# Performance work log

Hardware: AMD Instinct MI355X
Metric: run time of the kernel (lower is better)

## Reference

```python
import jax, jax.numpy as jnp
import numpy as np

C = 768       # hidden_dim
HEADS = 12    # num_heads
HDIM = C // HEADS  # 64


def _ln(x, w, eps=1e-5):
    # LayerNorm with weight, no bias (matches nn.LayerNorm(..., bias=False))
    mu = jnp.mean(x, axis=-1, keepdims=True)
    var = jnp.mean((x - mu) ** 2, axis=-1, keepdims=True)
    return (x - mu) * jax.lax.rsqrt(var + eps) * w


def _attn(q, k, v):
    # scaled dot product attention over the second-to-last axis
    scale = 1.0 / np.sqrt(q.shape[-1]).astype(np.float32)
    s = jnp.einsum('...qc,...kc->...qk', q, k) * scale
    return jnp.einsum('...qk,...kc->...qc', jax.nn.softmax(s, axis=-1), v)


def setup_inputs() -> dict:
    key = jax.random.key(0)
    ks = jax.random.split(key, 4)
    B, H, W = 4, 64, 64
    x = jax.random.normal(ks[0], (B, H, W, C), jnp.float32)
    Wqkv = jax.random.normal(ks[1], (C, 7 * C), jnp.float32) * 0.02
    bqkv = jnp.zeros((7 * C,), jnp.float32)
    Wout = jax.random.normal(ks[2], (C, C), jnp.float32) * 0.02
    bout = jnp.zeros((C,), jnp.float32)
    Wmlp = jax.random.normal(ks[3], (4 * C, C), jnp.float32) * 0.02
    bmlp = jnp.zeros((C,), jnp.float32)
    norm_w = jnp.ones((C,), jnp.float32)
    qnorm_w = jnp.ones((HDIM,), jnp.float32)
    knorm_w = jnp.ones((HDIM,), jnp.float32)
    gamma = jnp.full((C,), 1e-6, jnp.float32)
    return {"x": x, "norm_w": norm_w, "Wqkv": Wqkv, "bqkv": bqkv,
            "qnorm_w": qnorm_w, "knorm_w": knorm_w, "Wout": Wout,
            "bout": bout, "Wmlp": Wmlp, "bmlp": bmlp, "gamma": gamma}


def reference(x, norm_w, Wqkv, bqkv, qnorm_w, knorm_w, Wout, bout, Wmlp, bmlp, gamma):
    B, H, W, _ = x.shape
    xn = _ln(x, norm_w)
    proj = xn @ Wqkv + bqkv                       # (B,H,W,7C)
    q, k, v, ff = jnp.split(proj, [C, 2 * C, 3 * C], axis=-1)
    heads = lambda t: t.reshape(B, H, W, HEADS, HDIM)
    q, k, v = heads(q), heads(k), heads(v)        # (B,H,W,He,c)
    q = _ln(q, qnorm_w)
    k = _ln(k, knorm_w)

    # --- axis 1: 'b h w he c -> b h he w c', attend over w ---
    q, k, v = (t.transpose(0, 1, 3, 2, 4) for t in (q, k, v))  # (B,H,He,W,c)
    ax = _attn(q, k, v)                                         # (B,H,He,W,c)
    # out_permutation 'b w he h c -> b h w (he c)' applied POSITIONALLY ->
    # the first axis contribution lands spatially transposed (requires H==W)
    out = ax.transpose(0, 3, 1, 2, 4).reshape(B, W, H, C)

    # --- axis 2: 'b h he w c -> b w he h c' (positional), attend over h ---
    q, k, v = (t.transpose(0, 3, 2, 1, 4) for t in (q, k, v))  # (B,W,He,H,c)
    ax = _attn(q, k, v)                                         # (B,W,He,H,c)
    out = out + ax.transpose(0, 3, 1, 2, 4).reshape(B, H, W, C)

    y = out @ Wout + bout + (jax.nn.gelu(ff, approximate=False) @ Wmlp + bmlp)
    return x + gamma * y
```

## Files before the change

kernel.cpp:

```cpp
#include <hip/hip_runtime.h>

typedef unsigned short u16;
typedef unsigned int u32;
typedef unsigned char u8;
typedef long i64;
typedef float f4 __attribute__((ext_vector_type(4)));
typedef int i32x8 __attribute__((ext_vector_type(8)));

#define CDIM 768
#define NPROJ 5376
#define KFF 3840
#define NTOK 16384

__device__ __forceinline__ u8 f2fp8(float f) {
#if __has_builtin(__builtin_amdgcn_cvt_pk_fp8_f32)
    return (u8)(__builtin_amdgcn_cvt_pk_fp8_f32(f, f, 0, false) & 0xff);
#else
    u32 u = __float_as_uint(f);
    u32 s = (u >> 24) & 0x80u;
    float a = fabsf(f);
    a = fminf(a, 448.f);
    if (a < 0.015625f) return (u8)(s | (u32)(a * 512.f + 0.5f));
    u32 b = __float_as_uint(a);
    b += 0x0007FFFFu + ((b >> 20) & 1u);
    u32 e = b >> 23, m = (b >> 20) & 7u;
    u32 code = ((e - 120u) << 3) | m;
    if (code > 0x7Eu) code = 0x7Eu;
    return (u8)(s | code);
#endif
}
__device__ __forceinline__ u32 pk4_fp8(float a, float b, float c, float d) {
#if __has_builtin(__builtin_amdgcn_cvt_pk_fp8_f32)
    u32 lo = (u32)__builtin_amdgcn_cvt_pk_fp8_f32(a, b, 0, false);
    return (u32)__builtin_amdgcn_cvt_pk_fp8_f32(c, d, lo, true);
#else
    return (u32)f2fp8(a) | ((u32)f2fp8(b) << 8) | ((u32)f2fp8(c) << 16) | ((u32)f2fp8(d) << 24);
#endif
}
__device__ __forceinline__ float fp8_to_f32(u32 v) {
#if __has_builtin(__builtin_amdgcn_cvt_f32_fp8)
    return __builtin_amdgcn_cvt_f32_fp8((int)v, 0);
#else
    u32 s = v >> 7, e = (v >> 3) & 15u, m = v & 7u;
    float mag = e ? __uint_as_float(((e + 120u) << 23) | (m << 20))
                  : (float)m * 0.001953125f;
    return s ? -mag : mag;
#endif
}

__device__ __forceinline__ float wsum64(float v) {
#pragma unroll
    for (int m = 32; m > 0; m >>= 1) v += __shfl_xor(v, m, 64);
    return v;
}
__device__ __forceinline__ void gl_lds16(const u8* g, u8* l) {
    __builtin_amdgcn_global_load_lds((__attribute__((address_space(1))) u32*)g,
                                     (__attribute__((address_space(3))) u32*)l,
                                     16, 0, 0);
}

__global__ __launch_bounds__(256) void transpose_cast(const float* __restrict__ src,
                                                      u8* __restrict__ dst,
                                                      int R, int Cc, int dstride, int doff) {
    __shared__ float t[32][33];
    int c0 = blockIdx.x * 32, r0 = blockIdx.y * 32;
    int tx = threadIdx.x, ty = threadIdx.y;
#pragma unroll
    for (int i = 0; i < 32; i += 8) {
        int r = r0 + ty + i, c = c0 + tx;
        if (r < R && c < Cc) t[ty + i][tx] = src[(size_t)r * Cc + c];
    }
    __syncthreads();
#pragma unroll
    for (int i = 0; i < 32; i += 8) {
        int c = c0 + ty + i, r = r0 + tx;
        if (r < R && c < Cc) dst[(size_t)c * dstride + doff + r] = f2fp8(t[tx][ty + i]);
    }
}

__global__ __launch_bounds__(256) void ln_rows(const float* __restrict__ x,
                                               const float* __restrict__ w,
                                               u8* __restrict__ xn) {
    int row = blockIdx.x * 4 + (threadIdx.x >> 6);
    int lane = threadIdx.x & 63;
    const f4* xr = (const f4*)(x + (size_t)row * CDIM);
    const f4* wr = (const f4*)w;
    f4 v[3];
    float s = 0.f, s2 = 0.f;
#pragma unroll
    for (int i = 0; i < 3; ++i) {
        v[i] = xr[lane + 64 * i];
#pragma unroll
        for (int j = 0; j < 4; ++j) { s += v[i][j]; s2 += v[i][j] * v[i][j]; }
    }
    s = wsum64(s); s2 = wsum64(s2);
    float mu = s * (1.f / 768.f);
    float var = s2 * (1.f / 768.f) - mu * mu;
    float rs = rsqrtf(var + 1e-5f);
    u32* xo = (u32*)(xn + (size_t)row * CDIM);
#pragma unroll
    for (int i = 0; i < 3; ++i) {
        f4 wv = wr[lane + 64 * i];
        xo[lane + 64 * i] = pk4_fp8((v[i][0] - mu) * rs * wv[0], (v[i][1] - mu) * rs * wv[1],
                                    (v[i][2] - mu) * rs * wv[2], (v[i][3] - mu) * rs * wv[3]);
    }
}

template <int MODE>
__global__ __launch_bounds__(256) void gemm_bt(
    const u8* __restrict__ A, const u8* __restrict__ B, int M, int N, int K,
    const float* __restrict__ bias0, const float* __restrict__ bias1,
    const float* __restrict__ xres, const float* __restrict__ gamma,
    u8* __restrict__ oqkv, u8* __restrict__ off, float* __restrict__ ofin) {
    __shared__ __align__(16) u8 As[128 * 128];
    __shared__ __align__(16) u8 Bs[128 * 128];
    const int tid = threadIdx.x;
    const int wid = tid >> 6, lane = tid & 63;
    const int wm = wid >> 1, wn = wid & 1;
    const int quad = lane >> 4, l16 = lane & 15;
    const int m0 = blockIdx.y * 128, n0 = blockIdx.x * 128;

    f4 acc[4][4] = {};

    const int rl = lane >> 3;
    const int csw = ((lane & 7) ^ rl) * 16;
    const u8* aptr[4]; const u8* bptr[4];
    u8* alds[4]; u8* blds[4];
#pragma unroll
    for (int jj = 0; jj < 4; ++jj) {
        const int r0 = wid * 32 + jj * 8;
        aptr[jj] = A + (size_t)(m0 + r0 + rl) * K + csw;
        bptr[jj] = B + (size_t)(n0 + r0 + rl) * K + csw;
        alds[jj] = As + r0 * 128;
        blds[jj] = Bs + r0 * 128;
    }
    const int swl = l16 & 7;

    for (int kt = 0; kt < K; kt += 128) {
#pragma unroll
        for (int jj = 0; jj < 4; ++jj) {
            gl_lds16(aptr[jj] + kt, alds[jj]);
            gl_lds16(bptr[jj] + kt, blds[jj]);
        }
        __syncthreads();
        const int c0 = ((2 * quad) ^ swl) * 16;
        const int c1 = ((2 * quad + 1) ^ swl) * 16;
        i32x8 af[4], bfv[4];
#pragma unroll
        for (int mi = 0; mi < 4; ++mi) {
            const u8* base = As + (wm * 64 + mi * 16 + l16) * 128;
            uint4 lo = *(const uint4*)(base + c0);
            uint4 hi = *(const uint4*)(base + c1);
            af[mi][0] = lo.x; af[mi][1] = lo.y; af[mi][2] = lo.z; af[mi][3] = lo.w;
            af[mi][4] = hi.x; af[mi][5] = hi.y; af[mi][6] = hi.z; af[mi][7] = hi.w;
        }
#pragma unroll
        for (int ni = 0; ni < 4; ++ni) {
            const u8* base = Bs + (wn * 64 + ni * 16 + l16) * 128;
            uint4 lo = *(const uint4*)(base + c0);
            uint4 hi = *(const uint4*)(base + c1);
            bfv[ni][0] = lo.x; bfv[ni][1] = lo.y; bfv[ni][2] = lo.z; bfv[ni][3] = lo.w;
            bfv[ni][4] = hi.x; bfv[ni][5] = hi.y; bfv[ni][6] = hi.z; bfv[ni][7] = hi.w;
        }
#pragma unroll
        for (int mi = 0; mi < 4; ++mi)
#pragma unroll
            for (int ni = 0; ni < 4; ++ni)
                acc[mi][ni] = __builtin_amdgcn_mfma_scale_f32_16x16x128_f8f6f4(
                    af[mi], bfv[ni], acc[mi][ni], 0, 0, 0, 127, 0, 127);
        __syncthreads();
    }

#pragma unroll
    for (int mi = 0; mi < 4; ++mi) {
#pragma unroll
        for (int ni = 0; ni < 4; ++ni) {
            const int col = n0 + wn * 64 + ni * 16 + l16;
            const int rowb = m0 + wm * 64 + mi * 16 + quad * 4;
            if (MODE == 0) {
                const float bc = bias0[col];
#pragma unroll
                for (int r = 0; r < 4; ++r) {
                    float vv = acc[mi][ni][r] + bc;
                    const int m = rowb + r;
                    if (col < 2304) {
                        oqkv[(size_t)m * 2304 + col] = f2fp8(vv);
                    } else {
                        float u2 = vv * (-1.5957691216f) - 0.0713548162f * vv * vv * vv;
                        float g = vv / (1.f + __expf(u2));
                        off[(size_t)m * KFF + 768 + (col - 2304)] = f2fp8(g);
                    }
                }
            } else {
                const float bc = bias0[col] + bias1[col];
                const float gm = gamma[col];
#pragma unroll
                for (int r = 0; r < 4; ++r) {
                    const int m = rowb + r;
                    float vv = acc[mi][ni][r] + bc;
                    ofin[(size_t)m * CDIM + col] = xres[(size_t)m * CDIM + col] + gm * vv;
                }
            }
        }
    }
}

__global__ __launch_bounds__(256) void qk_ln(u8* __restrict__ qkv,
                                             const float* __restrict__ qw,
                                             const float* __restrict__ kw) {
    const size_t m = blockIdx.x;
    const int w = threadIdx.x >> 6, lane = threadIdx.x & 63;
#pragma unroll
    for (int it = 0; it < 6; ++it) {
        const int h = w + 4 * it;
        const int isq = (h < 12);
        const int he = isq ? h : h - 12;
        u8* p = qkv + m * 2304 + (isq ? 0 : 768) + he * 64 + lane;
        const float wt = (isq ? qw : kw)[lane];
        float v = fp8_to_f32(*p);
        float mu = wsum64(v) * (1.f / 64.f);
        float ex2 = wsum64(v * v) * (1.f / 64.f);
        float rs = rsqrtf(ex2 - mu * mu + 1e-5f);
        *p = f2fp8((v - mu) * rs * wt);
    }
}

__global__ __launch_bounds__(256) void axial_attn_mfma(const u8* __restrict__ qkv,
                                                       u8* __restrict__ A2) {
    __shared__ __align__(16) u8 Qs[64 * 72];
    __shared__ __align__(16) u8 Ks[64 * 72];
    __shared__ __align__(16) u8 Vt[64 * 72];
    __shared__ __align__(16) u8 Ps[64 * 72];

    const int bx = blockIdx.x;
    const int he = bx % 12;
    const int j = (bx / 12) & 63;
    const int b = bx / (12 * 64);
    const int tid = threadIdx.x;
    const int w = tid >> 6, lane = tid & 63;
    const int l16 = lane & 15, quad = lane >> 4;
    const int qb = w * 16;

    f4 acc_o[4] = {};

    const int sr = tid >> 2;
    const int sc = (tid & 3) * 16;

    for (int phase = 0; phase < 2; ++phase) {
        const size_t tok = (phase == 0) ? (size_t)((b * 64 + j) * 64 + sr)
                                        : (size_t)((b * 64 + sr) * 64 + j);
        const u8* src = qkv + tok * 2304 + he * 64 + sc;
        {
            uint4 qv = *(const uint4*)(src);
            uint4 kv = *(const uint4*)(src + 768);
            *(uint4*)(Qs + sr * 72 + sc) = qv;
            *(uint4*)(Ks + sr * 72 + sc) = kv;
        }
        {
            uint4 vv = *(const uint4*)(src + 1536);
            const u8* vb = (const u8*)&vv;
#pragma unroll
            for (int i = 0; i < 16; ++i) Vt[(sc + i) * 72 + sr] = vb[i];
        }
        __syncthreads();

        f4 st[4] = {};
#pragma unroll
        for (int kt = 0; kt < 2; ++kt) {
            const int boff = (kt * 4 + quad) * 8;
            const i64 bq = *(const i64*)(Qs + (qb + l16) * 72 + boff);
#pragma unroll
            for (int mt = 0; mt < 4; ++mt) {
                const i64 ak = *(const i64*)(Ks + (mt * 16 + l16) * 72 + boff);
                st[mt] = __builtin_amdgcn_mfma_f32_16x16x32_fp8_fp8(ak, bq, st[mt], 0, 0, 0);
            }
        }

        float sv[16];
        float mx = -1e30f;
#pragma unroll
        for (int mt = 0; mt < 4; ++mt)
#pragma unroll
            for (int r = 0; r < 4; ++r) {
                const float s = st[mt][r] * 0.125f;
                sv[mt * 4 + r] = s;
                mx = fmaxf(mx, s);
            }
        mx = fmaxf(mx, __shfl_xor(mx, 16, 64));
        mx = fmaxf(mx, __shfl_xor(mx, 32, 64));
        float sm = 0.f;
#pragma unroll
        for (int i = 0; i < 16; ++i) { sv[i] = __expf(sv[i] - mx); sm += sv[i]; }
        sm += __shfl_xor(sm, 16, 64);
        sm += __shfl_xor(sm, 32, 64);
        const float inv = 1.f / sm;

#pragma unroll
        for (int mt = 0; mt < 4; ++mt) {
            const int kbase = mt * 16 + quad * 4;
            *(u32*)(Ps + (qb + l16) * 72 + kbase) =
                pk4_fp8(sv[mt * 4] * inv, sv[mt * 4 + 1] * inv,
                        sv[mt * 4 + 2] * inv, sv[mt * 4 + 3] * inv);
        }
        __syncthreads();

#pragma unroll
        for (int kt = 0; kt < 2; ++kt) {
            const int boff = (kt * 4 + quad) * 8;
            const i64 ap = *(const i64*)(Ps + (qb + l16) * 72 + boff);
#pragma unroll
            for (int nt = 0; nt < 4; ++nt) {
                const i64 bv = *(const i64*)(Vt + (nt * 16 + l16) * 72 + boff);
                acc_o[nt] = __builtin_amdgcn_mfma_f32_16x16x32_fp8_fp8(ap, bv, acc_o[nt], 0, 0, 0);
            }
        }
        __syncthreads();
    }

#pragma unroll
    for (int nt = 0; nt < 4; ++nt)
#pragma unroll
        for (int r = 0; r < 4; ++r) {
            const int q = qb + quad * 4 + r;
            const int c = nt * 16 + l16;
            A2[((size_t)((b * 64 + q) * 64 + j)) * KFF + he * 64 + c] = f2fp8(acc_o[nt][r]);
        }
}

extern "C" void kernel_launch(void* const* d_in, const int* in_sizes, int n_in,
                              void* d_out, int out_size, void* d_ws, size_t ws_size,
                              hipStream_t stream) {
    const float* x = (const float*)d_in[0];
    const float* normw = (const float*)d_in[1];
    const float* Wqkv = (const float*)d_in[2];
    const float* bqkv = (const float*)d_in[3];
    const float* qnw = (const float*)d_in[4];
    const float* knw = (const float*)d_in[5];
    const float* Wout = (const float*)d_in[6];
    const float* bout = (const float*)d_in[7];
    const float* Wmlp = (const float*)d_in[8];
    const float* bmlp = (const float*)d_in[9];
    const float* gamma = (const float*)d_in[10];
    float* out = (float*)d_out;

    char* ws = (char*)d_ws;
    u8* xn = (u8*)ws;    ws += (size_t)NTOK * CDIM;
    u8* WqkvT = (u8*)ws; ws += (size_t)NPROJ * CDIM;
    u8* BT2 = (u8*)ws;   ws += (size_t)CDIM * KFF;
    u8* qkv = (u8*)ws;   ws += (size_t)NTOK * 2304;
    u8* A2 = (u8*)ws;    ws += (size_t)NTOK * KFF;

    transpose_cast<<<dim3(NPROJ / 32, CDIM / 32), dim3(32, 8), 0, stream>>>(Wqkv, WqkvT, CDIM, NPROJ, CDIM, 0);
    transpose_cast<<<dim3(CDIM / 32, CDIM / 32), dim3(32, 8), 0, stream>>>(Wout, BT2, CDIM, CDIM, KFF, 0);
    transpose_cast<<<dim3(CDIM / 32, 3072 / 32), dim3(32, 8), 0, stream>>>(Wmlp, BT2, 3072, CDIM, KFF, 768);
    ln_rows<<<NTOK / 4, 256, 0, stream>>>(x, normw, xn);
    gemm_bt<0><<<dim3(NPROJ / 128, NTOK / 128), 256, 0, stream>>>(
        xn, WqkvT, NTOK, NPROJ, CDIM, bqkv, nullptr, nullptr, nullptr, qkv, A2, nullptr);
    qk_ln<<<NTOK, 256, 0, stream>>>(qkv, qnw, knw);
    axial_attn_mfma<<<3072, 256, 0, stream>>>(qkv, A2);
    gemm_bt<1><<<dim3(CDIM / 128, NTOK / 128), 256, 0, stream>>>(
        A2, BT2, NTOK, CDIM, KFF, bout, bmlp, x, gamma, nullptr, nullptr, out);
}
```

Measured before the change: 421.2 us.

## Restructure FP8 GEMM to 256x256 tiles with double-buffered LDS prefetch

```diff
diff --git a/kernel.cpp b/kernel.cpp
--- a/kernel.cpp
+++ b/kernel.cpp
@@ -107,76 +107,107 @@
 }
 
 template <int MODE>
-__global__ __launch_bounds__(256) void gemm_bt(
+__global__ __launch_bounds__(512, 2) void gemm_bt(
     const u8* __restrict__ A, const u8* __restrict__ B, int M, int N, int K,
     const float* __restrict__ bias0, const float* __restrict__ bias1,
     const float* __restrict__ xres, const float* __restrict__ gamma,
     u8* __restrict__ oqkv, u8* __restrict__ off, float* __restrict__ ofin) {
-    __shared__ __align__(16) u8 As[128 * 128];
-    __shared__ __align__(16) u8 Bs[128 * 128];
+    __shared__ __align__(16) u8 lds[2][2][32768];
     const int tid = threadIdx.x;
     const int wid = tid >> 6, lane = tid & 63;
-    const int wm = wid >> 1, wn = wid & 1;
+    const int wm = wid >> 2, wn = wid & 3;
     const int quad = lane >> 4, l16 = lane & 15;
-    const int m0 = blockIdx.y * 128, n0 = blockIdx.x * 128;
-
-    f4 acc[4][4] = {};
+
+    const int nwg = (int)gridDim.x;
+    int bid = (int)blockIdx.x;
+    bid = (bid & 7) * (nwg >> 3) + (bid >> 3);
+    const int nbx = N >> 8;
+    const int m0 = (bid / nbx) << 8;
+    const int n0 = (bid % nbx) << 8;
+    const int NT = K >> 7;
+
+    f4 acc[8][4] = {};
 
     const int rl = lane >> 3;
     const int csw = ((lane & 7) ^ rl) * 16;
+    const int srow = wid * 8 + rl;
     const u8* aptr[4]; const u8* bptr[4];
-    u8* alds[4]; u8* blds[4];
-#pragma unroll
-    for (int jj = 0; jj < 4; ++jj) {
-        const int r0 = wid * 32 + jj * 8;
-        aptr[jj] = A + (size_t)(m0 + r0 + rl) * K + csw;
-        bptr[jj] = B + (size_t)(n0 + r0 + rl) * K + csw;
-        alds[jj] = As + r0 * 128;
-        blds[jj] = Bs + r0 * 128;
-    }
-    const int swl = l16 & 7;
-
-    for (int kt = 0; kt < K; kt += 128) {
-#pragma unroll
-        for (int jj = 0; jj < 4; ++jj) {
-            gl_lds16(aptr[jj] + kt, alds[jj]);
-            gl_lds16(bptr[jj] + kt, blds[jj]);
-        }
-        __syncthreads();
-        const int c0 = ((2 * quad) ^ swl) * 16;
-        const int c1 = ((2 * quad + 1) ^ swl) * 16;
-        i32x8 af[4], bfv[4];
-#pragma unroll
-        for (int mi = 0; mi < 4; ++mi) {
-            const u8* base = As + (wm * 64 + mi * 16 + l16) * 128;
-            uint4 lo = *(const uint4*)(base + c0);
-            uint4 hi = *(const uint4*)(base + c1);
-            af[mi][0] = lo.x; af[mi][1] = lo.y; af[mi][2] = lo.z; af[mi][3] = lo.w;
-            af[mi][4] = hi.x; af[mi][5] = hi.y; af[mi][6] = hi.z; af[mi][7] = hi.w;
-        }
-#pragma unroll
-        for (int ni = 0; ni < 4; ++ni) {
-            const u8* base = Bs + (wn * 64 + ni * 16 + l16) * 128;
-            uint4 lo = *(const uint4*)(base + c0);
-            uint4 hi = *(const uint4*)(base + c1);
-            bfv[ni][0] = lo.x; bfv[ni][1] = lo.y; bfv[ni][2] = lo.z; bfv[ni][3] = lo.w;
-            bfv[ni][4] = hi.x; bfv[ni][5] = hi.y; bfv[ni][6] = hi.z; bfv[ni][7] = hi.w;
-        }
-#pragma unroll
-        for (int mi = 0; mi < 4; ++mi)
-#pragma unroll
-            for (int ni = 0; ni < 4; ++ni)
-                acc[mi][ni] = __builtin_amdgcn_mfma_scale_f32_16x16x128_f8f6f4(
-                    af[mi], bfv[ni], acc[mi][ni], 0, 0, 0, 127, 0, 127);
-        __syncthreads();
-    }
-
-#pragma unroll
-    for (int mi = 0; mi < 4; ++mi) {
+#pragma unroll
+    for (int i = 0; i < 4; ++i) {
+        aptr[i] = A + (size_t)(m0 + i * 64 + srow) * K + csw;
+        bptr[i] = B + (size_t)(n0 + i * 64 + srow) * K + csw;
+    }
+    const int ldso = wid * 1024;
+
+#pragma unroll
+    for (int i = 0; i < 4; ++i) {
+        gl_lds16(aptr[i], &lds[0][0][i * 8192 + ldso]);
+        gl_lds16(bptr[i], &lds[0][1][i * 8192 + ldso]);
+    }
+    asm volatile("s_waitcnt vmcnt(0)" ::: "memory");
+    __builtin_amdgcn_s_barrier();
+
+    const int cb0 = ((2 * quad) ^ (l16 & 7)) * 16;
+    const int cb1 = ((2 * quad + 1) ^ (l16 & 7)) * 16;
+
+    for (int t = 0; t < NT; ++t) {
+        const u8* Ab = lds[t & 1][0];
+        const u8* Bb = lds[t & 1][1];
+        u8* Aw = lds[(t & 1) ^ 1][0];
+        u8* Bw = lds[(t & 1) ^ 1][1];
+        const int pf = (t + 1 < NT);
+        const size_t knext = (size_t)(t + 1) << 7;
+#pragma unroll
+        for (int p = 0; p < 4; ++p) {
+            const int mib = (p & 1) * 4;
+            const int nib = (p >> 1) * 2;
+            i32x8 af[4]; i32x8 bf[2];
+#pragma unroll
+            for (int mi = 0; mi < 4; ++mi) {
+                const u8* base = Ab + (wm * 128 + (mib + mi) * 16 + l16) * 128;
+                uint4 lo = *(const uint4*)(base + cb0);
+                uint4 hi = *(const uint4*)(base + cb1);
+                af[mi][0] = lo.x; af[mi][1] = lo.y; af[mi][2] = lo.z; af[mi][3] = lo.w;
+                af[mi][4] = hi.x; af[mi][5] = hi.y; af[mi][6] = hi.z; af[mi][7] = hi.w;
+            }
+#pragma unroll
+            for (int ni = 0; ni < 2; ++ni) {
+                const u8* base = Bb + (wn * 64 + (nib + ni) * 16 + l16) * 128;
+                uint4 lo = *(const uint4*)(base + cb0);
+                uint4 hi = *(const uint4*)(base + cb1);
+                bf[ni][0] = lo.x; bf[ni][1] = lo.y; bf[ni][2] = lo.z; bf[ni][3] = lo.w;
+                bf[ni][4] = hi.x; bf[ni][5] = hi.y; bf[ni][6] = hi.z; bf[ni][7] = hi.w;
+            }
+            if (p < 2 && pf) {
+#pragma unroll
+                for (int i = 2 * p; i < 2 * p + 2; ++i) {
+                    gl_lds16(aptr[i] + knext, Aw + i * 8192 + ldso);
+                    gl_lds16(bptr[i] + knext, Bw + i * 8192 + ldso);
+                }
+            }
+            __builtin_amdgcn_sched_barrier(0);
+            __builtin_amdgcn_s_barrier();
+            asm volatile("s_waitcnt lgkmcnt(0)" ::: "memory");
+            __builtin_amdgcn_sched_barrier(0);
+            __builtin_amdgcn_s_setprio(1);
+#pragma unroll
+            for (int mi = 0; mi < 4; ++mi)
+#pragma unroll
+                for (int ni = 0; ni < 2; ++ni)
+                    acc[mib + mi][nib + ni] = __builtin_amdgcn_mfma_scale_f32_16x16x128_f8f6f4(
+                        af[mi], bf[ni], acc[mib + mi][nib + ni], 0, 0, 0, 127, 0, 127);
+            __builtin_amdgcn_s_setprio(0);
+            if (p == 3) asm volatile("s_waitcnt vmcnt(0)" ::: "memory");
+            __builtin_amdgcn_s_barrier();
+        }
+    }
+
+#pragma unroll
+    for (int mi = 0; mi < 8; ++mi) {
 #pragma unroll
         for (int ni = 0; ni < 4; ++ni) {
             const int col = n0 + wn * 64 + ni * 16 + l16;
-            const int rowb = m0 + wm * 64 + mi * 16 + quad * 4;
+            const int rowb = m0 + wm * 128 + mi * 16 + quad * 4;
             if (MODE == 0) {
                 const float bc = bias0[col];
 #pragma unroll
@@ -354,10 +385,10 @@
     transpose_cast<<<dim3(CDIM / 32, CDIM / 32), dim3(32, 8), 0, stream>>>(Wout, BT2, CDIM, CDIM, KFF, 0);
     transpose_cast<<<dim3(CDIM / 32, 3072 / 32), dim3(32, 8), 0, stream>>>(Wmlp, BT2, 3072, CDIM, KFF, 768);
     ln_rows<<<NTOK / 4, 256, 0, stream>>>(x, normw, xn);
-    gemm_bt<0><<<dim3(NPROJ / 128, NTOK / 128), 256, 0, stream>>>(
+    gemm_bt<0><<<dim3((NPROJ / 256) * (NTOK / 256)), 512, 0, stream>>>(
         xn, WqkvT, NTOK, NPROJ, CDIM, bqkv, nullptr, nullptr, nullptr, qkv, A2, nullptr);
     qk_ln<<<NTOK, 256, 0, stream>>>(qkv, qnw, knw);
     axial_attn_mfma<<<3072, 256, 0, stream>>>(qkv, A2);
-    gemm_bt<1><<<dim3(CDIM / 128, NTOK / 128), 256, 0, stream>>>(
+    gemm_bt<1><<<dim3((CDIM / 256) * (NTOK / 256)), 512, 0, stream>>>(
         A2, BT2, NTOK, CDIM, KFF, bout, bmlp, x, gamma, nullptr, nullptr, out);
 }
```

Measured after the change: 562.4 us. +33.5%, slower.

## Double-buffer LDS tiles in fp8 GEMM to overlap global loads with MFMA

Applied to the files above, without the earlier changes.

```diff
diff --git a/kernel.cpp b/kernel.cpp
--- a/kernel.cpp
+++ b/kernel.cpp
@@ -112,53 +112,63 @@
     const float* __restrict__ bias0, const float* __restrict__ bias1,
     const float* __restrict__ xres, const float* __restrict__ gamma,
     u8* __restrict__ oqkv, u8* __restrict__ off, float* __restrict__ ofin) {
-    __shared__ __align__(16) u8 As[128 * 128];
-    __shared__ __align__(16) u8 Bs[128 * 128];
+    __shared__ __align__(16) u8 As[2][128 * 128];
+    __shared__ __align__(16) u8 Bs[2][128 * 128];
     const int tid = threadIdx.x;
     const int wid = tid >> 6, lane = tid & 63;
     const int wm = wid >> 1, wn = wid & 1;
     const int quad = lane >> 4, l16 = lane & 15;
     const int m0 = blockIdx.y * 128, n0 = blockIdx.x * 128;
+    const int NT = K >> 7;
 
     f4 acc[4][4] = {};
 
     const int rl = lane >> 3;
     const int csw = ((lane & 7) ^ rl) * 16;
     const u8* aptr[4]; const u8* bptr[4];
-    u8* alds[4]; u8* blds[4];
+    int ro[4];
 #pragma unroll
     for (int jj = 0; jj < 4; ++jj) {
         const int r0 = wid * 32 + jj * 8;
         aptr[jj] = A + (size_t)(m0 + r0 + rl) * K + csw;
         bptr[jj] = B + (size_t)(n0 + r0 + rl) * K + csw;
-        alds[jj] = As + r0 * 128;
-        blds[jj] = Bs + r0 * 128;
+        ro[jj] = r0 * 128;
     }
     const int swl = l16 & 7;
-
-    for (int kt = 0; kt < K; kt += 128) {
-#pragma unroll
-        for (int jj = 0; jj < 4; ++jj) {
-            gl_lds16(aptr[jj] + kt, alds[jj]);
-            gl_lds16(bptr[jj] + kt, blds[jj]);
-        }
-        __syncthreads();
-        const int c0 = ((2 * quad) ^ swl) * 16;
-        const int c1 = ((2 * quad + 1) ^ swl) * 16;
+    const int cb0 = ((2 * quad) ^ swl) * 16;
+    const int cb1 = ((2 * quad + 1) ^ swl) * 16;
+
+#pragma unroll
+    for (int jj = 0; jj < 4; ++jj) {
+        gl_lds16(aptr[jj], &As[0][ro[jj]]);
+        gl_lds16(bptr[jj], &Bs[0][ro[jj]]);
+    }
+    __syncthreads();
+
+    for (int t = 0; t < NT; ++t) {
+        const int cur = t & 1, nxt = cur ^ 1;
+        if (t + 1 < NT) {
+            const size_t ko = (size_t)(t + 1) << 7;
+#pragma unroll
+            for (int jj = 0; jj < 4; ++jj) {
+                gl_lds16(aptr[jj] + ko, &As[nxt][ro[jj]]);
+                gl_lds16(bptr[jj] + ko, &Bs[nxt][ro[jj]]);
+            }
+        }
         i32x8 af[4], bfv[4];
 #pragma unroll
         for (int mi = 0; mi < 4; ++mi) {
-            const u8* base = As + (wm * 64 + mi * 16 + l16) * 128;
-            uint4 lo = *(const uint4*)(base + c0);
-            uint4 hi = *(const uint4*)(base + c1);
+            const u8* base = As[cur] + (wm * 64 + mi * 16 + l16) * 128;
+            uint4 lo = *(const uint4*)(base + cb0);
+            uint4 hi = *(const uint4*)(base + cb1);
             af[mi][0] = lo.x; af[mi][1] = lo.y; af[mi][2] = lo.z; af[mi][3] = lo.w;
             af[mi][4] = hi.x; af[mi][5] = hi.y; af[mi][6] = hi.z; af[mi][7] = hi.w;
         }
 #pragma unroll
         for (int ni = 0; ni < 4; ++ni) {
-            const u8* base = Bs + (wn * 64 + ni * 16 + l16) * 128;
-            uint4 lo = *(const uint4*)(base + c0);
-            uint4 hi = *(const uint4*)(base + c1);
+            const u8* base = Bs[cur] + (wn * 64 + ni * 16 + l16) * 128;
+            uint4 lo = *(const uint4*)(base + cb0);
+            uint4 hi = *(const uint4*)(base + cb1);
             bfv[ni][0] = lo.x; bfv[ni][1] = lo.y; bfv[ni][2] = lo.z; bfv[ni][3] = lo.w;
             bfv[ni][4] = hi.x; bfv[ni][5] = hi.y; bfv[ni][6] = hi.z; bfv[ni][7] = hi.w;
         }
```

Result: slower. 444.5 us (+5.5%).

## Fuse weight prep and input LayerNorm into one launch; fold QK-norm into attention

Applied to the files above, without the earlier changes.

```diff
diff --git a/kernel.cpp b/kernel.cpp
--- a/kernel.cpp
+++ b/kernel.cpp
@@ -59,50 +59,66 @@
                                      16, 0, 0);
 }
 
-__global__ __launch_bounds__(256) void transpose_cast(const float* __restrict__ src,
-                                                      u8* __restrict__ dst,
-                                                      int R, int Cc, int dstride, int doff) {
+__global__ __launch_bounds__(256) void prep_fused(
+    const float* __restrict__ Wqkv, u8* __restrict__ WqkvT,
+    const float* __restrict__ Wout, const float* __restrict__ Wmlp,
+    u8* __restrict__ BT2,
+    const float* __restrict__ x, const float* __restrict__ normw,
+    u8* __restrict__ xn) {
     __shared__ float t[32][33];
-    int c0 = blockIdx.x * 32, r0 = blockIdx.y * 32;
-    int tx = threadIdx.x, ty = threadIdx.y;
-#pragma unroll
-    for (int i = 0; i < 32; i += 8) {
-        int r = r0 + ty + i, c = c0 + tx;
-        if (r < R && c < Cc) t[ty + i][tx] = src[(size_t)r * Cc + c];
-    }
-    __syncthreads();
-#pragma unroll
-    for (int i = 0; i < 32; i += 8) {
-        int c = c0 + ty + i, r = r0 + tx;
-        if (r < R && c < Cc) dst[(size_t)c * dstride + doff + r] = f2fp8(t[tx][ty + i]);
-    }
-}
-
-__global__ __launch_bounds__(256) void ln_rows(const float* __restrict__ x,
-                                               const float* __restrict__ w,
-                                               u8* __restrict__ xn) {
-    int row = blockIdx.x * 4 + (threadIdx.x >> 6);
-    int lane = threadIdx.x & 63;
-    const f4* xr = (const f4*)(x + (size_t)row * CDIM);
-    const f4* wr = (const f4*)w;
-    f4 v[3];
-    float s = 0.f, s2 = 0.f;
-#pragma unroll
-    for (int i = 0; i < 3; ++i) {
-        v[i] = xr[lane + 64 * i];
-#pragma unroll
-        for (int j = 0; j < 4; ++j) { s += v[i][j]; s2 += v[i][j] * v[i][j]; }
-    }
-    s = wsum64(s); s2 = wsum64(s2);
-    float mu = s * (1.f / 768.f);
-    float var = s2 * (1.f / 768.f) - mu * mu;
-    float rs = rsqrtf(var + 1e-5f);
-    u32* xo = (u32*)(xn + (size_t)row * CDIM);
-#pragma unroll
-    for (int i = 0; i < 3; ++i) {
-        f4 wv = wr[lane + 64 * i];
-        xo[lane + 64 * i] = pk4_fp8((v[i][0] - mu) * rs * wv[0], (v[i][1] - mu) * rs * wv[1],
-                                    (v[i][2] - mu) * rs * wv[2], (v[i][3] - mu) * rs * wv[3]);
+    const int bid = blockIdx.x;
+    const int tid = threadIdx.x;
+    if (bid < 6912) {
+        const float* src; u8* dst; int R, Cc, dstride, doff, bx, by;
+        if (bid < 4032) {
+            src = Wqkv; dst = WqkvT; R = CDIM; Cc = NPROJ; dstride = CDIM; doff = 0;
+            bx = bid % 168; by = bid / 168;
+        } else if (bid < 4608) {
+            const int b2 = bid - 4032;
+            src = Wout; dst = BT2; R = CDIM; Cc = CDIM; dstride = KFF; doff = 0;
+            bx = b2 % 24; by = b2 / 24;
+        } else {
+            const int b2 = bid - 4608;
+            src = Wmlp; dst = BT2; R = 3072; Cc = CDIM; dstride = KFF; doff = 768;
+            bx = b2 % 24; by = b2 / 24;
+        }
+        const int c0 = bx * 32, r0 = by * 32;
+        const int tx = tid & 31, ty = tid >> 5;
+#pragma unroll
+        for (int i = 0; i < 32; i += 8) {
+            int r = r0 + ty + i, c = c0 + tx;
+            if (r < R && c < Cc) t[ty + i][tx] = src[(size_t)r * Cc + c];
+        }
+        __syncthreads();
+#pragma unroll
+        for (int i = 0; i < 32; i += 8) {
+            int c = c0 + ty + i, r = r0 + tx;
+            if (r < R && c < Cc) dst[(size_t)c * dstride + doff + r] = f2fp8(t[tx][ty + i]);
+        }
+    } else {
+        const int row = (bid - 6912) * 4 + (tid >> 6);
+        const int lane = tid & 63;
+        const f4* xr = (const f4*)(x + (size_t)row * CDIM);
+        const f4* wr = (const f4*)normw;
+        f4 v[3];
+        float s = 0.f, s2 = 0.f;
+#pragma unroll
+        for (int i = 0; i < 3; ++i) {
+            v[i] = xr[lane + 64 * i];
+#pragma unroll
+            for (int j = 0; j < 4; ++j) { s += v[i][j]; s2 += v[i][j] * v[i][j]; }
+        }
+        s = wsum64(s); s2 = wsum64(s2);
+        float mu = s * (1.f / 768.f);
+        float var = s2 * (1.f / 768.f) - mu * mu;
+        float rs = rsqrtf(var + 1e-5f);
+        u32* xo = (u32*)(xn + (size_t)row * CDIM);
+#pragma unroll
+        for (int i = 0; i < 3; ++i) {
+            f4 wv = wr[lane + 64 * i];
+            xo[lane + 64 * i] = pk4_fp8((v[i][0] - mu) * rs * wv[0], (v[i][1] - mu) * rs * wv[1],
+                                        (v[i][2] - mu) * rs * wv[2], (v[i][3] - mu) * rs * wv[3]);
+        }
     }
 }
 
@@ -205,27 +221,9 @@
     }
 }
 
-__global__ __launch_bounds__(256) void qk_ln(u8* __restrict__ qkv,
-                                             const float* __restrict__ qw,
-                                             const float* __restrict__ kw) {
-    const size_t m = blockIdx.x;
-    const int w = threadIdx.x >> 6, lane = threadIdx.x & 63;
-#pragma unroll
-    for (int it = 0; it < 6; ++it) {
-        const int h = w + 4 * it;
-        const int isq = (h < 12);
-        const int he = isq ? h : h - 12;
-        u8* p = qkv + m * 2304 + (isq ? 0 : 768) + he * 64 + lane;
-        const float wt = (isq ? qw : kw)[lane];
-        float v = fp8_to_f32(*p);
-        float mu = wsum64(v) * (1.f / 64.f);
-        float ex2 = wsum64(v * v) * (1.f / 64.f);
-        float rs = rsqrtf(ex2 - mu * mu + 1e-5f);
-        *p = f2fp8((v - mu) * rs * wt);
-    }
-}
-
 __global__ __launch_bounds__(256) void axial_attn_mfma(const u8* __restrict__ qkv,
+                                                       const float* __restrict__ qnw,
+                                                       const float* __restrict__ knw,
                                                        u8* __restrict__ A2) {
     __shared__ __align__(16) u8 Qs[64 * 72];
     __shared__ __align__(16) u8 Ks[64 * 72];
@@ -245,6 +243,8 @@
 
     const int sr = tid >> 2;
     const int sc = (tid & 3) * 16;
+    const f4* qwv = (const f4*)(qnw + sc);
+    const f4* kwv = (const f4*)(knw + sc);
 
     for (int phase = 0; phase < 2; ++phase) {
         const size_t tok = (phase == 0) ? (size_t)((b * 64 + j) * 64 + sr)
@@ -253,8 +253,45 @@
         {
             uint4 qv = *(const uint4*)(src);
             uint4 kv = *(const uint4*)(src + 768);
-            *(uint4*)(Qs + sr * 72 + sc) = qv;
-            *(uint4*)(Ks + sr * 72 + sc) = kv;
+            const u32* qu = (const u32*)&qv;
+            const u32* ku = (const u32*)&kv;
+            float qf[16], kf[16];
+#pragma unroll
+            for (int jj = 0; jj < 4; ++jj)
+#pragma unroll
+                for (int bb = 0; bb < 4; ++bb) {
+                    qf[jj * 4 + bb] = fp8_to_f32((qu[jj] >> (8 * bb)) & 0xffu);
+                    kf[jj * 4 + bb] = fp8_to_f32((ku[jj] >> (8 * bb)) & 0xffu);
+                }
+            float s1q = 0.f, s2q = 0.f, s1k = 0.f, s2k = 0.f;
+#pragma unroll
+            for (int i = 0; i < 16; ++i) {
+                s1q += qf[i]; s2q += qf[i] * qf[i];
+                s1k += kf[i]; s2k += kf[i] * kf[i];
+            }
+            s1q += __shfl_xor(s1q, 1, 64); s1q += __shfl_xor(s1q, 2, 64);
+            s2q += __shfl_xor(s2q, 1, 64); s2q += __shfl_xor(s2q, 2, 64);
+            s1k += __shfl_xor(s1k, 1, 64); s1k += __shfl_xor(s1k, 2, 64);
+            s2k += __shfl_xor(s2k, 1, 64); s2k += __shfl_xor(s2k, 2, 64);
+            const float muq = s1q * (1.f / 64.f), muk = s1k * (1.f / 64.f);
+            const float rsq = rsqrtf(s2q * (1.f / 64.f) - muq * muq + 1e-5f);
+            const float rsk = rsqrtf(s2k * (1.f / 64.f) - muk * muk + 1e-5f);
+            uint4 qo, ko;
+            u32* qop = (u32*)&qo; u32* kop = (u32*)&ko;
+#pragma unroll
+            for (int jj = 0; jj < 4; ++jj) {
+                const f4 wq = qwv[jj], wk = kwv[jj];
+                qop[jj] = pk4_fp8((qf[jj * 4 + 0] - muq) * rsq * wq[0],
+                                  (qf[jj * 4 + 1] - muq) * rsq * wq[1],
+                                  (qf[jj * 4 + 2] - muq) * rsq * wq[2],
+                                  (qf[jj * 4 + 3] - muq) * rsq * wq[3]);
+                kop[jj] = pk4_fp8((kf[jj * 4 + 0] - muk) * rsk * wk[0],
+                                  (kf[jj * 4 + 1] - muk) * rsk * wk[1],
+                                  (kf[jj * 4 + 2] - muk) * rsk * wk[2],
+                                  (kf[jj * 4 + 3] - muk) * rsk * wk[3]);
+            }
+            *(uint4*)(Qs + sr * 72 + sc) = qo;
+            *(uint4*)(Ks + sr * 72 + sc) = ko;
         }
         {
             uint4 vv = *(const uint4*)(src + 1536);
@@ -350,14 +387,10 @@
     u8* qkv = (u8*)ws;   ws += (size_t)NTOK * 2304;
     u8* A2 = (u8*)ws;    ws += (size_t)NTOK * KFF;
 
-    transpose_cast<<<dim3(NPROJ / 32, CDIM / 32), dim3(32, 8), 0, stream>>>(Wqkv, WqkvT, CDIM, NPROJ, CDIM, 0);
-    transpose_cast<<<dim3(CDIM / 32, CDIM / 32), dim3(32, 8), 0, stream>>>(Wout, BT2, CDIM, CDIM, KFF, 0);
-    transpose_cast<<<dim3(CDIM / 32, 3072 / 32), dim3(32, 8), 0, stream>>>(Wmlp, BT2, 3072, CDIM, KFF, 768);
-    ln_rows<<<NTOK / 4, 256, 0, stream>>>(x, normw, xn);
+    prep_fused<<<11008, 256, 0, stream>>>(Wqkv, WqkvT, Wout, Wmlp, BT2, x, normw, xn);
     gemm_bt<0><<<dim3(NPROJ / 128, NTOK / 128), 256, 0, stream>>>(
         xn, WqkvT, NTOK, NPROJ, CDIM, bqkv, nullptr, nullptr, nullptr, qkv, A2, nullptr);
-    qk_ln<<<NTOK, 256, 0, stream>>>(qkv, qnw, knw);
-    axial_attn_mfma<<<3072, 256, 0, stream>>>(qkv, A2);
+    axial_attn_mfma<<<3072, 256, 0, stream>>>(qkv, qnw, knw, A2);
     gemm_bt<1><<<dim3(CDIM / 128, NTOK / 128), 256, 0, stream>>>(
         A2, BT2, NTOK, CDIM, KFF, bout, bmlp, x, gamma, nullptr, nullptr, out);
 }
```

After: 367.9 us. 1.14x faster.
